# Optimization experiments

Measured on AMD Instinct MI355X. Metric: run time of the kernel, lower is better.

Reference implementation:

```python
import jax, jax.numpy as jnp
import numpy as np

NUM_ANCHORS = 3


def _decode_scale(output, thresh, anchor, step):
    # output: [B, C, H, W] with C = 3*(5+num_classes); anchor: [3, 2]
    B, C, H, W = output.shape
    o = jnp.transpose(output, (0, 2, 3, 1)).reshape(B, H, W, NUM_ANCHORS, -1)
    conf = o[..., 0]
    mask = conf > thresh  # data-dependent filter -> expressed as dense mask (jit-safe)
    gy = jnp.arange(H, dtype=o.dtype)[None, :, None, None]  # index[:,1]
    gx = jnp.arange(W, dtype=o.dtype)[None, None, :, None]  # index[:,2]
    cx = (gx + o[..., 1]) * step
    cy = (gy + o[..., 2]) * step
    w = anchor[:, 0] * jnp.exp(o[..., 3])  # broadcast over anchor axis a
    h = anchor[:, 1] * jnp.exp(o[..., 4])
    x1 = cx - w * 0.5
    y1 = cy - h * 0.5
    x2 = x1 + w
    y2 = y1 + h
    cls = jax.lax.stop_gradient(jnp.argmax(o[..., 5:], axis=-1).astype(o.dtype))
    out = jnp.stack([conf, x1, y1, x2, y2, cls], axis=-1)  # [B,H,W,3,6]
    out = jnp.where(mask[..., None], out, jnp.zeros((), o.dtype))
    return out.reshape(-1, 6)


def setup_inputs() -> dict:
    key = jax.random.key(0)
    k13, k26, k52, ka = jax.random.split(key, 4)
    B, C = 32, 255  # 3 anchors * (5 + 80 classes)
    return {
        "output13": jax.random.normal(k13, (B, C, 13, 13), dtype=jnp.float32),
        "output26": jax.random.normal(k26, (B, C, 26, 26), dtype=jnp.float32),
        "output52": jax.random.normal(k52, (B, C, 52, 52), dtype=jnp.float32),
        "anchors": jax.random.uniform(ka, (3, 3, 2), dtype=jnp.float32),
    }


def reference(output13, output26, output52, anchors):
    out13 = _decode_scale(output13, 0.5, anchors[0], 32.0)
    out26 = _decode_scale(output26, 0.5, anchors[1], 16.0)
    out52 = _decode_scale(output52, 0.9, anchors[2], 8.0)
    return jnp.concatenate([out13, out26, out52], axis=0)
```

## Files before the change

### kernel.cpp

```cpp
#include <hip/hip_runtime.h>
#include <hip/hip_bf16.h>
#include <float.h>


#define NUM_B 32
#define NUM_CLS 80
#define CH 255

#define R13 (NUM_B * 13 * 13 * 3)
#define R26 (NUM_B * 26 * 26 * 3)
#define CUM13 R13
#define CUM26 (R13 + R26)

#define NBLK13 (NUM_B * 3)
#define NBLK26 (NUM_B * 3)
#define NBLK52 (NUM_B * 3 * 3)

template <int H, int AOFF>
__device__ __forceinline__ void decode_tile_s(
    const float* __restrict__ in,
    const float* __restrict__ anchors,
    float thresh, float step,
    int idx,
    float* __restrict__ outs)
{
    constexpr int W  = H;
    constexpr int HW = H * W;

    const int a = idx % 3;
    const int b = idx / 3;

    const int hw = threadIdx.x;
    if (hw >= HW) return;

    const float* p = in + ((size_t)(b * CH + a * 85)) * HW + hw;

    const float conf = p[0];
    const float tx   = p[1 * HW];
    const float ty   = p[2 * HW];
    const float tw   = p[3 * HW];
    const float th   = p[4 * HW];

    const float* pc = p + 5 * HW;
    float best = -FLT_MAX;
    int   bi   = 0;
    #pragma unroll
    for (int c0 = 0; c0 < NUM_CLS; c0 += 16) {
        float v[16];
        #pragma unroll
        for (int k = 0; k < 16; ++k)
            v[k] = pc[(size_t)(c0 + k) * HW];
        #pragma unroll
        for (int k = 0; k < 16; ++k)
            if (v[k] > best) { best = v[k]; bi = c0 + k; }
    }

    const int wi = hw % W;
    const int hi = hw / W;

    const float cx = ((float)wi + tx) * step;
    const float cy = ((float)hi + ty) * step;
    const float aw = anchors[AOFF + a * 2 + 0] * __expf(tw);
    const float ah = anchors[AOFF + a * 2 + 1] * __expf(th);

    const float x1 = cx - aw * 0.5f;
    const float y1 = cy - ah * 0.5f;
    const float x2 = x1 + aw;
    const float y2 = y1 + ah;

    const bool m = conf > thresh;
    float2* o2 = (float2*)(outs + ((size_t)(b * HW + hw) * 3 + a) * 6);
    o2[0] = m ? make_float2(conf, x1)      : make_float2(0.f, 0.f);
    o2[1] = m ? make_float2(y1, x2)        : make_float2(0.f, 0.f);
    o2[2] = m ? make_float2(y2, (float)bi) : make_float2(0.f, 0.f);
}

template <int H, int AOFF, int NTILE>
__device__ __forceinline__ void decode_tile_v4(
    const float* __restrict__ in,
    const float* __restrict__ anchors,
    float thresh, float step,
    int idx,
    float* __restrict__ outs)
{
    constexpr int W   = H;
    constexpr int HW  = H * W;
    constexpr int HW4 = HW / 4;

    const int tile = idx % NTILE;
    const int ba   = idx / NTILE;
    const int a    = ba % 3;
    const int b    = ba / 3;

    const int q = tile * 256 + threadIdx.x;
    if (q >= HW4) return;

    const float4* p = (const float4*)(in + ((size_t)(b * CH + a * 85)) * HW) + q;

    const float4 conf4 = p[0];
    const float4 tx4   = p[1 * HW4];
    const float4 ty4   = p[2 * HW4];
    const float4 tw4   = p[3 * HW4];
    const float4 th4   = p[4 * HW4];

    const float4* pc = p + 5 * HW4;
    float best[4] = {-FLT_MAX, -FLT_MAX, -FLT_MAX, -FLT_MAX};
    int   bi[4]   = {0, 0, 0, 0};
    #pragma unroll
    for (int c0 = 0; c0 < NUM_CLS; c0 += 20) {
        float4 v[20];
        #pragma unroll
        for (int k = 0; k < 20; ++k)
            v[k] = pc[(size_t)(c0 + k) * HW4];
        #pragma unroll
        for (int k = 0; k < 20; ++k) {
            const float vv[4] = {v[k].x, v[k].y, v[k].z, v[k].w};
            #pragma unroll
            for (int i = 0; i < 4; ++i)
                if (vv[i] > best[i]) { best[i] = vv[i]; bi[i] = c0 + k; }
        }
    }

    const float aw_a = anchors[AOFF + a * 2 + 0];
    const float ah_a = anchors[AOFF + a * 2 + 1];

    const float cf[4] = {conf4.x, conf4.y, conf4.z, conf4.w};
    const float tx[4] = {tx4.x, tx4.y, tx4.z, tx4.w};
    const float ty[4] = {ty4.x, ty4.y, ty4.z, ty4.w};
    const float tw[4] = {tw4.x, tw4.y, tw4.z, tw4.w};
    const float th[4] = {th4.x, th4.y, th4.z, th4.w};

    #pragma unroll
    for (int i = 0; i < 4; ++i) {
        const int hw = 4 * q + i;
        const int wi = hw % W;
        const int hi = hw / W;

        const float cx = ((float)wi + tx[i]) * step;
        const float cy = ((float)hi + ty[i]) * step;
        const float aw = aw_a * __expf(tw[i]);
        const float ah = ah_a * __expf(th[i]);

        const float x1 = cx - aw * 0.5f;
        const float y1 = cy - ah * 0.5f;
        const float x2 = x1 + aw;
        const float y2 = y1 + ah;

        const bool m = cf[i] > thresh;
        float2* o2 = (float2*)(outs + ((size_t)(b * HW + hw) * 3 + a) * 6);
        o2[0] = m ? make_float2(cf[i], x1)        : make_float2(0.f, 0.f);
        o2[1] = m ? make_float2(y1, x2)           : make_float2(0.f, 0.f);
        o2[2] = m ? make_float2(y2, (float)bi[i]) : make_float2(0.f, 0.f);
    }
}

__global__ __launch_bounds__(256) void detector_decode(
    const float* __restrict__ in13,
    const float* __restrict__ in26,
    const float* __restrict__ in52,
    const float* __restrict__ anchors,
    float* __restrict__ out)
{
    const int bid = blockIdx.x;
    if (bid < NBLK13) {
        decode_tile_s<13, 0>(in13, anchors, 0.5f, 32.0f, bid, out);
    } else if (bid < NBLK13 + NBLK26) {
        decode_tile_v4<26, 6, 1>(in26, anchors, 0.5f, 16.0f, bid - NBLK13,
                                 out + (size_t)CUM13 * 6);
    } else {
        decode_tile_v4<52, 12, 3>(in52, anchors, 0.9f, 8.0f,
                                  bid - (NBLK13 + NBLK26),
                                  out + (size_t)CUM26 * 6);
    }
}

extern "C" void kernel_launch(void* const* d_in, const int* in_sizes, int n_in,
                              void* d_out, int out_size, void* d_ws, size_t ws_size,
                              hipStream_t stream) {
    const float* in13    = (const float*)d_in[0];
    const float* in26    = (const float*)d_in[1];
    const float* in52    = (const float*)d_in[2];
    const float* anchors = (const float*)d_in[3];
    float* out = (float*)d_out;

    const int blocks = NBLK13 + NBLK26 + NBLK52;
    detector_decode<<<blocks, 256, 0, stream>>>(in13, in26, in52, anchors, out);
}
```

Measured before the change: 30.86 us.

## Split class argmax across lane groups with wave shuffle reduction for 26/52 scales

Each wavefront now handles 16 float4 positions, with four lane groups each scanning 20 of the 80 classes. Partial argmax results are combined with xor shuffles, keeping the lowest index on ties. Block counts grow so the 26 and 52 scales spread over many more blocks, giving more memory-level parallelism and shorter per-thread serial load chains. The cost is wasted lanes on tail tiles, extra shuffle work, and three quarters of the lanes idling during the box decode and store.

```diff
diff --git a/kernel.cpp b/kernel.cpp
--- a/kernel.cpp
+++ b/kernel.cpp
@@ -13,8 +13,8 @@
 #define CUM26 (R13 + R26)
 
 #define NBLK13 (NUM_B * 3)
-#define NBLK26 (NUM_B * 3)
-#define NBLK52 (NUM_B * 3 * 3)
+#define NBLK26 (NUM_B * 3 * 3)
+#define NBLK52 (NUM_B * 3 * 11)
 
 template <int H, int AOFF>
 __device__ __forceinline__ void decode_tile_s(
@@ -76,7 +76,7 @@
 }
 
 template <int H, int AOFF, int NTILE>
-__device__ __forceinline__ void decode_tile_v4(
+__device__ __forceinline__ void decode_tile_v4cs(
     const float* __restrict__ in,
     const float* __restrict__ anchors,
     float thresh, float step,
@@ -92,34 +92,59 @@
     const int a    = ba % 3;
     const int b    = ba / 3;
 
-    const int q = tile * 256 + threadIdx.x;
-    if (q >= HW4) return;
-
-    const float4* p = (const float4*)(in + ((size_t)(b * CH + a * 85)) * HW) + q;
-
+    const int lane = threadIdx.x & 63;
+    const int wv   = threadIdx.x >> 6;
+    const int cc   = lane >> 4;
+    const int ql   = lane & 15;
+
+    const int qbase = tile * 64 + wv * 16;
+    if (qbase >= HW4) return;
+
+    const int  q   = qbase + ql;
+    const bool act = (q < HW4);
+    const int  qc  = act ? q : (HW4 - 1);
+
+    const float4* slab =
+        (const float4*)(in + ((size_t)(b * CH + a * 85)) * HW);
+
+    const float4* p = slab + qc;
     const float4 conf4 = p[0];
     const float4 tx4   = p[1 * HW4];
     const float4 ty4   = p[2 * HW4];
     const float4 tw4   = p[3 * HW4];
     const float4 th4   = p[4 * HW4];
 
-    const float4* pc = p + 5 * HW4;
+    const float4* pc = slab + (size_t)(5 + cc * 20) * HW4 + qc;
     float best[4] = {-FLT_MAX, -FLT_MAX, -FLT_MAX, -FLT_MAX};
     int   bi[4]   = {0, 0, 0, 0};
     #pragma unroll
-    for (int c0 = 0; c0 < NUM_CLS; c0 += 20) {
-        float4 v[20];
-        #pragma unroll
-        for (int k = 0; k < 20; ++k)
+    for (int c0 = 0; c0 < 20; c0 += 10) {
+        float4 v[10];
+        #pragma unroll
+        for (int k = 0; k < 10; ++k)
             v[k] = pc[(size_t)(c0 + k) * HW4];
         #pragma unroll
-        for (int k = 0; k < 20; ++k) {
+        for (int k = 0; k < 10; ++k) {
             const float vv[4] = {v[k].x, v[k].y, v[k].z, v[k].w};
             #pragma unroll
             for (int i = 0; i < 4; ++i)
-                if (vv[i] > best[i]) { best[i] = vv[i]; bi[i] = c0 + k; }
+                if (vv[i] > best[i]) { best[i] = vv[i]; bi[i] = cc * 20 + c0 + k; }
         }
     }
+
+    #pragma unroll
+    for (int off = 16; off <= 32; off <<= 1) {
+        #pragma unroll
+        for (int i = 0; i < 4; ++i) {
+            const float ob  = __shfl_xor(best[i], off, 64);
+            const int   obi = __shfl_xor(bi[i],   off, 64);
+            if (ob > best[i] || (ob == best[i] && obi < bi[i])) {
+                best[i] = ob; bi[i] = obi;
+            }
+        }
+    }
+
+    if (cc != 0 || !act) return;
 
     const float aw_a = anchors[AOFF + a * 2 + 0];
     const float ah_a = anchors[AOFF + a * 2 + 1];
@@ -132,7 +157,7 @@
 
     #pragma unroll
     for (int i = 0; i < 4; ++i) {
-        const int hw = 4 * q + i;
+        const int hw = 4 * qc + i;
         const int wi = hw % W;
         const int hi = hw / W;
 
@@ -148,9 +173,9 @@
 
         const bool m = cf[i] > thresh;
         float2* o2 = (float2*)(outs + ((size_t)(b * HW + hw) * 3 + a) * 6);
-        o2[0] = m ? make_float2(cf[i], x1)        : make_float2(0.f, 0.f);
-        o2[1] = m ? make_float2(y1, x2)           : make_float2(0.f, 0.f);
-        o2[2] = m ? make_float2(y2, (float)bi[i]) : make_float2(0.f, 0.f);
+        o2[0] = m ? make_float2(cf[i], x1)         : make_float2(0.f, 0.f);
+        o2[1] = m ? make_float2(y1, x2)            : make_float2(0.f, 0.f);
+        o2[2] = m ? make_float2(y2, (float)bi[i])  : make_float2(0.f, 0.f);
     }
 }
 
@@ -165,12 +190,12 @@
     if (bid < NBLK13) {
         decode_tile_s<13, 0>(in13, anchors, 0.5f, 32.0f, bid, out);
     } else if (bid < NBLK13 + NBLK26) {
-        decode_tile_v4<26, 6, 1>(in26, anchors, 0.5f, 16.0f, bid - NBLK13,
-                                 out + (size_t)CUM13 * 6);
+        decode_tile_v4cs<26, 6, 3>(in26, anchors, 0.5f, 16.0f, bid - NBLK13,
+                                   out + (size_t)CUM13 * 6);
     } else {
-        decode_tile_v4<52, 12, 3>(in52, anchors, 0.9f, 8.0f,
-                                  bid - (NBLK13 + NBLK26),
-                                  out + (size_t)CUM26 * 6);
+        decode_tile_v4cs<52, 12, 11>(in52, anchors, 0.9f, 8.0f,
+                                     bid - (NBLK13 + NBLK26),
+                                     out + (size_t)CUM26 * 6);
     }
 }
 
```

New measurement: 28.76 us. 6.8% less time.
